# Kernel optimization log

Hardware: AMD Instinct MI355X
Metric: run time of the kernel (lower is better)

Reference implementation:

```python
import jax, jax.numpy as jnp
import numpy as np

ITER_STEPS = 2


def setup_inputs() -> dict:
    key = jax.random.key(0)
    ks = jax.random.split(key, 9)
    B, N, D, E = 64, 256, 512, 10  # batch, nodes, node_dim, edge types
    node = jax.random.normal(ks[0], (B, N, D), dtype=jnp.float32)
    node_mask = jax.random.randint(ks[1], (B, N), 0, 2).astype(jnp.int32)
    adj = jax.random.randint(ks[2], (E, B, N, N), 0, 2).astype(jnp.int32)
    s = 0.02
    W_nw = jax.random.normal(ks[3], (1, D), dtype=jnp.float32) * s   # node weight fc [out=1, in=D]
    b_nw = jnp.zeros((1,), dtype=jnp.float32)
    W_self = jax.random.normal(ks[4], (D, D), dtype=jnp.float32) * s
    b_self = jnp.zeros((D,), dtype=jnp.float32)
    W_edge = jax.random.normal(ks[5], (E, D, D), dtype=jnp.float32) * s  # per-edge-type Linear (no bias)
    return {"node": node, "W_nw": W_nw, "b_nw": b_nw, "W_self": W_self,
            "b_self": b_self, "W_edge": W_edge, "node_mask": node_mask, "adj": adj}


def reference(node, W_nw, b_nw, W_self, b_self, W_edge, node_mask, adj):
    # node: [B,N,D]; node_mask: [B,N] int; adj: [E=10,B,N,N] int (binary)
    B, N, D = node.shape
    m = node_mask.astype(node.dtype)
    eye = jnp.eye(N, dtype=node.dtype)
    # dd_graph = mask outer-product with zeroed diagonal: [B,N,N]
    dd = m[:, None, :] * m[:, :, None] * (1.0 - eye)
    graphs = dd[None] * adj.astype(node.dtype)  # [E,B,N,N]
    # total neighbor count across all 10 edge types, clamped to >=1 (replace_masked_values)
    neigh = graphs.sum(axis=(0, 3))                       # [B,N]
    neigh = jnp.where(neigh >= 1.0, neigh, 1.0)
    all_weight = []
    for _ in range(ITER_STEPS):
        # (1) node relatedness gate
        w = jax.nn.sigmoid(node @ W_nw.T + b_nw)[..., 0]  # [B,N]
        all_weight.append(w)
        self_info = node @ W_self.T + b_self              # [B,N,D]
        # (2) per-edge-type projection + masked adjacency matmul, summed over edge types
        proj = jnp.einsum('bnk,edk->ebnd', node, W_edge)  # [E,B,N,D]
        masked_w = jnp.where(graphs != 0, w[None, :, None, :], 0.0)  # [E,B,N,N]
        agg = jnp.einsum('ebnm,ebmd->bnd', masked_w, proj)           # [B,N,D]
        # (3) update
        node = jax.nn.relu(self_info + agg / neigh[..., None])
    return node, jnp.stack(all_weight, axis=1)  # ([B,N,D], [B,ITER,N])
```

## Files before the change

kernel.cpp:

```cpp
#include <hip/hip_runtime.h>
#include <hip/hip_bf16.h>

#define BB 64
#define NN 256
#define DD 512
#define EE 10

typedef __bf16 bf16x8 __attribute__((ext_vector_type(8)));
typedef unsigned short ushort8v __attribute__((ext_vector_type(8)));
typedef unsigned int uint4v __attribute__((ext_vector_type(4)));
typedef unsigned int uint2v __attribute__((ext_vector_type(2)));
typedef float floatx4 __attribute__((ext_vector_type(4)));
typedef float floatx16 __attribute__((ext_vector_type(16)));

typedef __attribute__((address_space(3))) unsigned short lds_us;
typedef const __attribute__((address_space(1))) unsigned short glb_us;

__device__ __forceinline__ unsigned short f2b(float f) {
    union { float f; unsigned u; } x; x.f = f;
    unsigned r = x.u + 0x7FFFu + ((x.u >> 16) & 1u);
    return (unsigned short)(r >> 16);
}
__device__ __forceinline__ float b2f(unsigned short u) {
    union { unsigned u; float f; } x; x.u = ((unsigned)u) << 16;
    return x.f;
}
__device__ __forceinline__ unsigned pack_bf16(float a, float b) {
    union { float f; unsigned u; } xa, xb2; xa.f = a; xb2.f = b;
    return __builtin_amdgcn_perm(xa.u + 0x8000u, xb2.u + 0x8000u, 0x07060302u);
}

__global__ void k_wconv(const float* __restrict__ W_edge,
                        const float* __restrict__ W_self,
                        unsigned short* __restrict__ Wf) {
    int t = blockIdx.x * 256 + threadIdx.x;
    int lane  = t & 63;
    int kstep = (t >> 6) & 31;
    int cfg   = (t >> 11) & 15;
    int e     = t >> 15;
    int dout = cfg * 32 + (lane & 31);
    int k    = kstep * 16 + (lane >> 5) * 8;
    const float* src = (e < EE) ? (W_edge + ((size_t)e * DD + dout) * DD + k)
                                : (W_self + (size_t)dout * DD + k);
    ushort8v o;
    #pragma unroll
    for (int j = 0; j < 8; j++) o[j] = f2b(src[j]);
    *(ushort8v*)(Wf + (size_t)t * 8) = o;
}

__global__ void k_graph(const int* __restrict__ adj, const int* __restrict__ mask,
                        unsigned* __restrict__ packed, float* __restrict__ recip) {
    int b = blockIdx.x >> 8;
    int n = blockIdx.x & 255;
    int lane = threadIdx.x & 63;
    int wv   = threadIdx.x >> 6;
    int m = wv * 64 + lane;
    int ok = (mask[b * NN + n] != 0) & (mask[b * NN + m] != 0) & (m != n);
    __shared__ int cnt_s[4];
    int total = 0;
    #pragma unroll
    for (int e = 0; e < EE; e++) {
        int a = adj[(((size_t)e * BB + b) * NN + n) * NN + m];
        int bit = ok & (a != 0);
        unsigned long long bal = __ballot(bit);
        if (lane == 0) {
            unsigned* dst = packed + (((size_t)e * BB + b) * NN + n) * 8 + wv * 2;
            dst[0] = (unsigned)bal;
            dst[1] = (unsigned)(bal >> 32);
        }
        total += bit;
    }
    for (int off = 32; off; off >>= 1) total += __shfl_down(total, off);
    if (lane == 0) cnt_s[wv] = total;
    __syncthreads();
    if (threadIdx.x == 0) {
        int c = cnt_s[0] + cnt_s[1] + cnt_s[2] + cnt_s[3];
        recip[b * NN + n] = 1.0f / (float)(c < 1 ? 1 : c);
    }
}

template<int TI>
__global__ __launch_bounds__(256)
void k_gt(const float* __restrict__ xf, const unsigned short* __restrict__ xbin,
          const float* __restrict__ W_nw, const float* __restrict__ b_nw,
          float* __restrict__ w_out, unsigned short* __restrict__ wTf,
          unsigned short* __restrict__ xb0) {
    int bid = blockIdx.x;
    int b  = bid >> 4;
    int ms = bid & 15;
    __shared__ float part[16][17];
    __shared__ float wsig[16];
    int t = threadIdx.x;
    int row = t >> 4;
    int seg = t & 15;
    size_t g = ((size_t)(b * NN + ms * 16 + row)) * DD + seg * 32;
    float s = 0.f;
    if (TI == 0) {
        const floatx4* xp = (const floatx4*)(xf + g);
        const floatx4* wp = (const floatx4*)(W_nw + seg * 32);
        #pragma unroll
        for (int k = 0; k < 4; k++) {
            floatx4 a = xp[2 * k], c4 = xp[2 * k + 1];
            floatx4 wa = wp[2 * k], wc = wp[2 * k + 1];
            ushort8v u;
            #pragma unroll
            for (int j = 0; j < 4; j++) {
                s += a[j] * wa[j] + c4[j] * wc[j];
                u[j] = f2b(a[j]); u[4 + j] = f2b(c4[j]);
            }
            *(ushort8v*)(xb0 + g + k * 8) = u;
        }
    } else {
        const ushort8v* xp = (const ushort8v*)(xbin + g);
        const float* wp = W_nw + seg * 32;
        #pragma unroll
        for (int k = 0; k < 4; k++) {
            ushort8v u = xp[k];
            #pragma unroll
            for (int j = 0; j < 8; j++) s += b2f(u[j]) * wp[k * 8 + j];
        }
    }
    part[row][seg] = s;
    __syncthreads();
    if (t < 16) {
        float tot = 0.f;
        #pragma unroll
        for (int i = 0; i < 16; i++) tot += part[t][i];
        float v = 1.f / (1.f + __expf(-(tot + b_nw[0])));
        wsig[t] = v;
        w_out[(b * 2 + TI) * NN + ms * 16 + t] = v;
    }
    __syncthreads();
    #pragma unroll
    for (int c = 0; c < 4; c++) {
        int slot = t + 256 * c;
        int dd_  = slot >> 6;
        int lane = slot & 63;
        int l31 = lane & 31, hi = lane >> 5;
        size_t xrow = ((size_t)(b * NN + ms * 16 + hi * 8)) * DD + dd_ * 32 + l31;
        float wv[8];
        ushort8v o;
        #pragma unroll
        for (int j = 0; j < 8; j++) {
            float xv = (TI == 0) ? xf[xrow + (size_t)j * DD] : b2f(xbin[xrow + (size_t)j * DD]);
            o[j] = f2b(xv * wsig[hi * 8 + j]);
        }
        (void)wv;
        *(ushort8v*)(wTf + ((((size_t)b * 16 + ms) * 16 + dd_) * 64 + lane) * 8) = o;
    }
}

template<int TI>
__global__ __launch_bounds__(512, 2)
void k2_heavy(const unsigned short* __restrict__ wTf,
              const unsigned short* __restrict__ xb,
              const unsigned short* __restrict__ Wf,
              const unsigned* __restrict__ packed,
              const float* __restrict__ recip,
              const float* __restrict__ b_self,
              unsigned short* __restrict__ out_bf16,
              float* __restrict__ out_f32) {
    __shared__ __attribute__((aligned(16))) unsigned short sWT[32 * 512];
    __shared__ __attribute__((aligned(16))) unsigned short sWf[2][32 * 512];
    __shared__ __attribute__((aligned(16))) unsigned short sTf[16 * 512];

    int bid = blockIdx.x;
    int ct = bid & 1;
    int p  = (bid >> 1) & 3;
    int b  = p * 16 + ((bid >> 3) & 15);
    int h  = bid >> 7;
    int w = threadIdx.x >> 6, lane = threadIdx.x & 63;
    int l31 = lane & 31, hi = lane >> 5;
    int s1_d  = w & 1;
    int s1_nb = w >> 1;
    int n1 = s1_nb * 32 + l31;
    float rn = recip[b * NN + h * 128 + n1];
    int nh2 = w & 1;
    int dh4 = w >> 1;

    floatx16 acc2[2][2];
    #pragma unroll
    for (int i = 0; i < 2; i++)
        #pragma unroll
        for (int jj = 0; jj < 2; jj++)
            #pragma unroll
            for (int q = 0; q < 16; q++) acc2[i][jj][q] = 0.f;

    auto stage_sWT = [&](int dc) {
        #pragma unroll
        for (int it = 0; it < 4; it++) {
            int c = it * 8 + w;
            const unsigned short* g = wTf +
                ((((size_t)b * 16 + (c >> 1)) * 16 + dc * 2 + (c & 1)) * 64 + lane) * 8;
            __builtin_amdgcn_global_load_lds((glb_us*)g, (lds_us*)&sWT[c * 512], 16, 0, 0);
        }
    };
    auto stage_sWf = [&](int e, int dc, int buf) {
        #pragma unroll
        for (int it = 0; it < 4; it++) {
            int c = it * 8 + w;
            const unsigned short* g = Wf +
                ((((size_t)e * 16 + ct * 8 + (c >> 2)) * 32 + dc * 4 + (c & 3)) * 64 + lane) * 8;
            __builtin_amdgcn_global_load_lds((glb_us*)g, (lds_us*)&sWf[buf][c * 512], 16, 0, 0);
        }
    };

    stage_sWT(0);
    stage_sWf(0, 0, 0);

    bf16x8 Bg[16];

    #pragma unroll 1
    for (int s = 0; s < 88; s++) {
        int e = s >> 3, dc = s & 7, cur = s & 1;
        asm volatile("s_waitcnt vmcnt(0)" ::: "memory");
        asm volatile("s_barrier" ::: "memory");
        if (s < 87) {
            int ns = s + 1;
            stage_sWf(ns >> 3, ns & 7, cur ^ 1);
        }
        if (e < EE) {
            if (dc == 0) {
                const uint4v* pp = (const uint4v*)(packed +
                    (((size_t)e * BB + b) * NN + h * 128 + n1) * 8);
                uint4v pa = pp[0], pb = pp[1];
                unsigned pw[8] = {pa[0], pa[1], pa[2], pa[3], pb[0], pb[1], pb[2], pb[3]};
                #pragma unroll
                for (int ks = 0; ks < 16; ks++) {
                    int byi = ks * 2 + hi;
                    unsigned byte = (pw[byi >> 2] >> ((byi & 3) * 8)) & 0xFFu;
                    uint4v av;
                    #pragma unroll
                    for (int pp2 = 0; pp2 < 4; pp2++) {
                        unsigned tt = (byte >> (2 * pp2)) & 3u;
                        unsigned u = (tt | (tt << 15)) & 0x10001u;
                        av[pp2] = u * 0x3F80u;
                    }
                    Bg[ks] = __builtin_bit_cast(bf16x8, av);
                }
            }
            floatx16 acc3a, acc3b;
            #pragma unroll
            for (int q = 0; q < 16; q++) { acc3a[q] = 0.f; acc3b[q] = 0.f; }
            #pragma unroll
            for (int ks = 0; ks < 8; ks++) {
                bf16x8 afrA = __builtin_bit_cast(bf16x8,
                    *(const ushort8v*)&sWT[((2 * ks) * 2 + s1_d) * 512 + lane * 8]);
                bf16x8 afrB = __builtin_bit_cast(bf16x8,
                    *(const ushort8v*)&sWT[((2 * ks + 1) * 2 + s1_d) * 512 + lane * 8]);
                acc3a = __builtin_amdgcn_mfma_f32_32x32x16_bf16(afrA, Bg[2 * ks],     acc3a, 0, 0, 0);
                acc3b = __builtin_amdgcn_mfma_f32_32x32x16_bf16(afrB, Bg[2 * ks + 1], acc3b, 0, 0, 0);
            }
            #pragma unroll
            for (int g = 0; g < 4; g++) {
                float v0 = (acc3a[g * 4 + 0] + acc3b[g * 4 + 0]) * rn;
                float v1 = (acc3a[g * 4 + 1] + acc3b[g * 4 + 1]) * rn;
                float v2 = (acc3a[g * 4 + 2] + acc3b[g * 4 + 2]) * rn;
                float v3 = (acc3a[g * 4 + 3] + acc3b[g * 4 + 3]) * rn;
                uint2v pk;
                pk[0] = pack_bf16(v1, v0);
                pk[1] = pack_bf16(v3, v2);
                int slot = (((s1_d * 2 + (g >> 1)) * 4 + s1_nb) * 64 + (g & 1) * 32 + l31);
                *(uint2v*)&sTf[slot * 8 + 4 * hi] = pk;
            }
            asm volatile("s_waitcnt lgkmcnt(0)" ::: "memory");
            asm volatile("s_barrier" ::: "memory");
            if (s + 1 < 80) stage_sWT((s + 1) & 7);
            #pragma unroll
            for (int kk = 0; kk < 4; kk++) {
                bf16x8 bfr[2];
                #pragma unroll
                for (int cb = 0; cb < 2; cb++)
                    bfr[cb] = __builtin_bit_cast(bf16x8, *(const ushort8v*)
                        &sWf[cur][(((dh4 * 2 + cb) * 4 + kk) * 64 + lane) * 8]);
                #pragma unroll
                for (int na = 0; na < 2; na++) {
                    int nb = nh2 * 2 + na;
                    bf16x8 afr = __builtin_bit_cast(bf16x8, *(const ushort8v*)
                        &sTf[((kk * 4 + nb) * 64 + lane) * 8]);
                    #pragma unroll
                    for (int cb = 0; cb < 2; cb++)
                        acc2[na][cb] = __builtin_amdgcn_mfma_f32_32x32x16_bf16(
                            afr, bfr[cb], acc2[na][cb], 0, 0, 0);
                }
            }
        } else {
            #pragma unroll
            for (int kk = 0; kk < 4; kk++) {
                bf16x8 bfr[2];
                #pragma unroll
                for (int cb = 0; cb < 2; cb++)
                    bfr[cb] = __builtin_bit_cast(bf16x8, *(const ushort8v*)
                        &sWf[cur][(((dh4 * 2 + cb) * 4 + kk) * 64 + lane) * 8]);
                #pragma unroll
                for (int na = 0; na < 2; na++) {
                    bf16x8 afr = __builtin_bit_cast(bf16x8, *(const ushort8v*)(xb +
                        ((size_t)(b * NN + h * 128 + nh2 * 64 + na * 32 + l31)) * DD +
                        dc * 64 + kk * 16 + hi * 8));
                    #pragma unroll
                    for (int cb = 0; cb < 2; cb++)
                        acc2[na][cb] = __builtin_amdgcn_mfma_f32_32x32x16_bf16(
                            afr, bfr[cb], acc2[na][cb], 0, 0, 0);
                }
            }
        }
    }
    #pragma unroll
    for (int cb = 0; cb < 2; cb++) {
        int col = ct * 256 + dh4 * 64 + cb * 32 + l31;
        float bs = b_self[col];
        #pragma unroll
        for (int na = 0; na < 2; na++) {
            #pragma unroll
            for (int rg = 0; rg < 16; rg++) {
                int row = h * 128 + nh2 * 64 + na * 32 + (rg & 3) + 8 * (rg >> 2) + 4 * hi;
                float v = acc2[na][cb][rg] + bs;
                v = v > 0.f ? v : 0.f;
                size_t gi = ((size_t)b * NN + row) * DD + col;
                if (TI == 0) out_bf16[gi] = f2b(v);
                else         out_f32[gi] = v;
            }
        }
    }
}

extern "C" void kernel_launch(void* const* d_in, const int* in_sizes, int n_in,
                              void* d_out, int out_size, void* d_ws, size_t ws_size,
                              hipStream_t stream) {
    const float* node   = (const float*)d_in[0];
    const float* W_nw   = (const float*)d_in[1];
    const float* b_nw   = (const float*)d_in[2];
    const float* W_self = (const float*)d_in[3];
    const float* b_self = (const float*)d_in[4];
    const float* W_edge = (const float*)d_in[5];
    const int*   mask   = (const int*)d_in[6];
    const int*   adj    = (const int*)d_in[7];
    float* out = (float*)d_out;
    float* out_w = out + (size_t)BB * NN * DD;

    char* ws = (char*)d_ws;
    size_t off = 0;
    unsigned short* Wf    = (unsigned short*)(ws + off); off += (size_t)11 * DD * DD * 2;
    unsigned short* wTf   = (unsigned short*)(ws + off); off += (size_t)BB * DD * NN * 2;
    unsigned short* xb0   = (unsigned short*)(ws + off); off += (size_t)BB * NN * DD * 2;
    unsigned short* xb1   = (unsigned short*)(ws + off); off += (size_t)BB * NN * DD * 2;
    unsigned*       packed= (unsigned*)(ws + off);       off += (size_t)EE * BB * NN * 8 * 4;
    float*          recip = (float*)(ws + off);          off += (size_t)BB * NN * 4;

    k_wconv<<<dim3(1408), dim3(256), 0, stream>>>(W_edge, W_self, Wf);
    k_graph<<<dim3(16384), dim3(256), 0, stream>>>(adj, mask, packed, recip);

    k_gt<0><<<dim3(1024), dim3(256), 0, stream>>>(node, nullptr, W_nw, b_nw, out_w, wTf, xb0);
    k2_heavy<0><<<dim3(256), dim3(512), 0, stream>>>(wTf, xb0, Wf, packed, recip, b_self, xb1, nullptr);

    k_gt<1><<<dim3(1024), dim3(256), 0, stream>>>(nullptr, xb1, W_nw, b_nw, out_w, wTf, nullptr);
    k2_heavy<1><<<dim3(256), dim3(512), 0, stream>>>(wTf, xb1, Wf, packed, recip, b_self, nullptr, out);
}
```

Before: 714.4 us.

## Restructure heavy kernel: per-block 64 nodes x full D, software-pipeline stage1/stage2

Retiles k2_heavy so each block handles 64 nodes of one batch across all 512 output columns instead of 128 nodes by 256 columns. The aggregation stage (adj x weighted-node) runs on 4 waves and writes a double-buffered sTf tile. The projection stage for the previous step overlaps it, which removes one barrier per step. Edge weights (Wf) are now read directly from global memory instead of being staged in LDS, cutting LDS use, at the cost of more global and L2 traffic and idle waves during stage one. The grid shape changes, and the launch code is not shown.

```diff
diff --git a/kernel.cpp b/kernel.cpp
--- a/kernel.cpp
+++ b/kernel.cpp
@@ -138,14 +138,12 @@
         int lane = slot & 63;
         int l31 = lane & 31, hi = lane >> 5;
         size_t xrow = ((size_t)(b * NN + ms * 16 + hi * 8)) * DD + dd_ * 32 + l31;
-        float wv[8];
         ushort8v o;
         #pragma unroll
         for (int j = 0; j < 8; j++) {
             float xv = (TI == 0) ? xf[xrow + (size_t)j * DD] : b2f(xbin[xrow + (size_t)j * DD]);
             o[j] = f2b(xv * wsig[hi * 8 + j]);
         }
-        (void)wv;
         *(ushort8v*)(wTf + ((((size_t)b * 16 + ms) * 16 + dd_) * 64 + lane) * 8) = o;
     }
 }
@@ -160,23 +158,18 @@
               const float* __restrict__ b_self,
               unsigned short* __restrict__ out_bf16,
               float* __restrict__ out_f32) {
-    __shared__ __attribute__((aligned(16))) unsigned short sWT[32 * 512];
-    __shared__ __attribute__((aligned(16))) unsigned short sWf[2][32 * 512];
-    __shared__ __attribute__((aligned(16))) unsigned short sTf[16 * 512];
+    __shared__ __attribute__((aligned(16))) unsigned short sWT[2][32 * 512];
+    __shared__ __attribute__((aligned(16))) unsigned short sTf[2][8 * 512];
 
     int bid = blockIdx.x;
-    int ct = bid & 1;
-    int p  = (bid >> 1) & 3;
-    int b  = p * 16 + ((bid >> 3) & 15);
-    int h  = bid >> 7;
+    int b  = bid & 63;
+    int nq = bid >> 6;
     int w = threadIdx.x >> 6, lane = threadIdx.x & 63;
     int l31 = lane & 31, hi = lane >> 5;
-    int s1_d  = w & 1;
-    int s1_nb = w >> 1;
-    int n1 = s1_nb * 32 + l31;
-    float rn = recip[b * NN + h * 128 + n1];
-    int nh2 = w & 1;
-    int dh4 = w >> 1;
+
+    int sd = w & 1, sn = (w >> 1) & 1;
+    int gn1 = nq * 64 + sn * 32 + l31;
+    float rn = recip[b * NN + gn1];
 
     floatx16 acc2[2][2];
     #pragma unroll
@@ -186,55 +179,47 @@
             #pragma unroll
             for (int q = 0; q < 16; q++) acc2[i][jj][q] = 0.f;
 
-    auto stage_sWT = [&](int dc) {
+    auto stage_sWT = [&](int dc, int buf) {
         #pragma unroll
         for (int it = 0; it < 4; it++) {
             int c = it * 8 + w;
             const unsigned short* g = wTf +
                 ((((size_t)b * 16 + (c >> 1)) * 16 + dc * 2 + (c & 1)) * 64 + lane) * 8;
-            __builtin_amdgcn_global_load_lds((glb_us*)g, (lds_us*)&sWT[c * 512], 16, 0, 0);
+            __builtin_amdgcn_global_load_lds((glb_us*)g, (lds_us*)&sWT[buf][c * 512], 16, 0, 0);
         }
     };
-    auto stage_sWf = [&](int e, int dc, int buf) {
-        #pragma unroll
-        for (int it = 0; it < 4; it++) {
-            int c = it * 8 + w;
-            const unsigned short* g = Wf +
-                ((((size_t)e * 16 + ct * 8 + (c >> 2)) * 32 + dc * 4 + (c & 3)) * 64 + lane) * 8;
-            __builtin_amdgcn_global_load_lds((glb_us*)g, (lds_us*)&sWf[buf][c * 512], 16, 0, 0);
-        }
-    };
-
-    stage_sWT(0);
-    stage_sWf(0, 0, 0);
+
+    stage_sWT(0, 0);
 
     bf16x8 Bg[16];
+    const unsigned short* WfL = Wf + lane * 8;
+    const unsigned short* xbL = xb + ((size_t)(b * NN + nq * 64 + l31)) * DD + hi * 8;
 
     #pragma unroll 1
-    for (int s = 0; s < 88; s++) {
-        int e = s >> 3, dc = s & 7, cur = s & 1;
-        asm volatile("s_waitcnt vmcnt(0)" ::: "memory");
-        asm volatile("s_barrier" ::: "memory");
-        if (s < 87) {
-            int ns = s + 1;
-            stage_sWf(ns >> 3, ns & 7, cur ^ 1);
-        }
-        if (e < EE) {
-            if (dc == 0) {
+    for (int s = 0; s < 89; s++) {
+        int cur = s & 1;
+        if (s <= 80) {
+            asm volatile("s_waitcnt vmcnt(0) lgkmcnt(0)" ::: "memory");
+            __builtin_amdgcn_s_barrier();
+            if (s + 1 < 80) stage_sWT((s + 1) & 7, (s + 1) & 1);
+        }
+        if (s < 80 && w < 4) {
+            int e = s >> 3;
+            if ((s & 7) == 0) {
                 const uint4v* pp = (const uint4v*)(packed +
-                    (((size_t)e * BB + b) * NN + h * 128 + n1) * 8);
+                    (((size_t)e * BB + b) * NN + gn1) * 8);
                 uint4v pa = pp[0], pb = pp[1];
                 unsigned pw[8] = {pa[0], pa[1], pa[2], pa[3], pb[0], pb[1], pb[2], pb[3]};
                 #pragma unroll
                 for (int ks = 0; ks < 16; ks++) {
                     int byi = ks * 2 + hi;
-                    unsigned byte = (pw[byi >> 2] >> ((byi & 3) * 8)) & 0xFFu;
+                    unsigned byte_ = (pw[byi >> 2] >> ((byi & 3) * 8)) & 0xFFu;
                     uint4v av;
                     #pragma unroll
-                    for (int pp2 = 0; pp2 < 4; pp2++) {
-                        unsigned tt = (byte >> (2 * pp2)) & 3u;
+                    for (int p2 = 0; p2 < 4; p2++) {
+                        unsigned tt = (byte_ >> (2 * p2)) & 3u;
                         unsigned u = (tt | (tt << 15)) & 0x10001u;
-                        av[pp2] = u * 0x3F80u;
+                        av[p2] = u * 0x3F80u;
                     }
                     Bg[ks] = __builtin_bit_cast(bf16x8, av);
                 }
@@ -245,9 +230,9 @@
             #pragma unroll
             for (int ks = 0; ks < 8; ks++) {
                 bf16x8 afrA = __builtin_bit_cast(bf16x8,
-                    *(const ushort8v*)&sWT[((2 * ks) * 2 + s1_d) * 512 + lane * 8]);
+                    *(const ushort8v*)&sWT[cur][((2 * ks) * 2 + sd) * 512 + lane * 8]);
                 bf16x8 afrB = __builtin_bit_cast(bf16x8,
-                    *(const ushort8v*)&sWT[((2 * ks + 1) * 2 + s1_d) * 512 + lane * 8]);
+                    *(const ushort8v*)&sWT[cur][((2 * ks + 1) * 2 + sd) * 512 + lane * 8]);
                 acc3a = __builtin_amdgcn_mfma_f32_32x32x16_bf16(afrA, Bg[2 * ks],     acc3a, 0, 0, 0);
                 acc3b = __builtin_amdgcn_mfma_f32_32x32x16_bf16(afrB, Bg[2 * ks + 1], acc3b, 0, 0, 0);
             }
@@ -260,61 +245,64 @@
                 uint2v pk;
                 pk[0] = pack_bf16(v1, v0);
                 pk[1] = pack_bf16(v3, v2);
-                int slot = (((s1_d * 2 + (g >> 1)) * 4 + s1_nb) * 64 + (g & 1) * 32 + l31);
-                *(uint2v*)&sTf[slot * 8 + 4 * hi] = pk;
-            }
-            asm volatile("s_waitcnt lgkmcnt(0)" ::: "memory");
-            asm volatile("s_barrier" ::: "memory");
-            if (s + 1 < 80) stage_sWT((s + 1) & 7);
-            #pragma unroll
-            for (int kk = 0; kk < 4; kk++) {
-                bf16x8 bfr[2];
+                int kk = sd * 2 + (g >> 1);
+                int slot = (kk * 2 + sn) * 64 + (g & 1) * 32 + l31;
+                *(uint2v*)&sTf[cur][slot * 8 + 4 * hi] = pk;
+            }
+        }
+        if (s >= 1) {
+            int q = s - 1;
+            int qe = q >> 3, qdc = q & 7, pb2 = q & 1;
+            if (qe < EE) {
+                const unsigned short* sTfL = &sTf[pb2][lane * 8];
                 #pragma unroll
-                for (int cb = 0; cb < 2; cb++)
-                    bfr[cb] = __builtin_bit_cast(bf16x8, *(const ushort8v*)
-                        &sWf[cur][(((dh4 * 2 + cb) * 4 + kk) * 64 + lane) * 8]);
+                for (int kk = 0; kk < 4; kk++) {
+                    bf16x8 afr[2];
+                    #pragma unroll
+                    for (int nb = 0; nb < 2; nb++)
+                        afr[nb] = __builtin_bit_cast(bf16x8,
+                            *(const ushort8v*)&sTfL[(kk * 2 + nb) * 512]);
+                    #pragma unroll
+                    for (int cb = 0; cb < 2; cb++) {
+                        bf16x8 bfr = __builtin_bit_cast(bf16x8, *(const ushort8v*)
+                            &WfL[(size_t)(((qe * 16 + w * 2 + cb) * 32 + qdc * 4 + kk)) * 512]);
+                        #pragma unroll
+                        for (int nb = 0; nb < 2; nb++)
+                            acc2[nb][cb] = __builtin_amdgcn_mfma_f32_32x32x16_bf16(
+                                afr[nb], bfr, acc2[nb][cb], 0, 0, 0);
+                    }
+                }
+            } else {
                 #pragma unroll
-                for (int na = 0; na < 2; na++) {
-                    int nb = nh2 * 2 + na;
-                    bf16x8 afr = __builtin_bit_cast(bf16x8, *(const ushort8v*)
-                        &sTf[((kk * 4 + nb) * 64 + lane) * 8]);
-                    #pragma unroll
-                    for (int cb = 0; cb < 2; cb++)
-                        acc2[na][cb] = __builtin_amdgcn_mfma_f32_32x32x16_bf16(
-                            afr, bfr[cb], acc2[na][cb], 0, 0, 0);
+                for (int kk = 0; kk < 4; kk++) {
+                    bf16x8 afr[2];
+                    #pragma unroll
+                    for (int nb = 0; nb < 2; nb++)
+                        afr[nb] = __builtin_bit_cast(bf16x8, *(const ushort8v*)
+                            &xbL[(size_t)nb * 32 * DD + qdc * 64 + kk * 16]);
+                    #pragma unroll
+                    for (int cb = 0; cb < 2; cb++) {
+                        bf16x8 bfr = __builtin_bit_cast(bf16x8, *(const ushort8v*)
+                            &WfL[(size_t)(((EE * 16 + w * 2 + cb) * 32 + qdc * 4 + kk)) * 512]);
+                        #pragma unroll
+                        for (int nb = 0; nb < 2; nb++)
+                            acc2[nb][cb] = __builtin_amdgcn_mfma_f32_32x32x16_bf16(
+                                afr[nb], bfr, acc2[nb][cb], 0, 0, 0);
+                    }
                 }
             }
-        } else {
-            #pragma unroll
-            for (int kk = 0; kk < 4; kk++) {
-                bf16x8 bfr[2];
-                #pragma unroll
-                for (int cb = 0; cb < 2; cb++)
-                    bfr[cb] = __builtin_bit_cast(bf16x8, *(const ushort8v*)
-                        &sWf[cur][(((dh4 * 2 + cb) * 4 + kk) * 64 + lane) * 8]);
-                #pragma unroll
-                for (int na = 0; na < 2; na++) {
-                    bf16x8 afr = __builtin_bit_cast(bf16x8, *(const ushort8v*)(xb +
-                        ((size_t)(b * NN + h * 128 + nh2 * 64 + na * 32 + l31)) * DD +
-                        dc * 64 + kk * 16 + hi * 8));
-                    #pragma unroll
-                    for (int cb = 0; cb < 2; cb++)
-                        acc2[na][cb] = __builtin_amdgcn_mfma_f32_32x32x16_bf16(
-                            afr, bfr[cb], acc2[na][cb], 0, 0, 0);
-                }
-            }
         }
     }
     #pragma unroll
     for (int cb = 0; cb < 2; cb++) {
-        int col = ct * 256 + dh4 * 64 + cb * 32 + l31;
+        int col = w * 64 + cb * 32 + l31;
         float bs = b_self[col];
         #pragma unroll
-        for (int na = 0; na < 2; na++) {
+        for (int nb = 0; nb < 2; nb++) {
             #pragma unroll
             for (int rg = 0; rg < 16; rg++) {
-                int row = h * 128 + nh2 * 64 + na * 32 + (rg & 3) + 8 * (rg >> 2) + 4 * hi;
-                float v = acc2[na][cb][rg] + bs;
+                int row = nq * 64 + nb * 32 + (rg & 3) + 8 * (rg >> 2) + 4 * hi;
+                float v = acc2[nb][cb][rg] + bs;
                 v = v > 0.f ? v : 0.f;
                 size_t gi = ((size_t)b * NN + row) * DD + col;
                 if (TI == 0) out_bf16[gi] = f2b(v);
```

Measured after the change: 748.8 us. 4.8% more time.
